# Kernel tuning notes

Hardware: AMD Instinct MI355X
Metric: run time of the kernel (lower is better)

## Reference

```python
import jax, jax.numpy as jnp
import numpy as np

B, N, C_IN, C_OUT = 2, 163842, 64, 64  # icosphere level-7 vertex count
K = 7  # 1-ring neighborhood size (center + 6 neighbors)


def setup_inputs() -> dict:
    key = jax.random.key(0)
    kx, kw, kb, kn = jax.random.split(key, 4)
    x = jax.random.normal(kx, (B, N, C_IN), dtype=jnp.float32)
    # nn.Linear(7*in_feats, out_feats): W is (out, 7*in), bias (out,)
    W = jax.random.normal(kw, (C_OUT, K * C_IN), dtype=jnp.float32) * (1.0 / np.sqrt(K * C_IN))
    b = jax.random.normal(kb, (C_OUT,), dtype=jnp.float32) * 0.01
    neigh_orders = jax.random.randint(kn, (K * N,), 0, N, dtype=jnp.int64)
    return {"x": x, "W": W, "b": b, "neigh_orders": neigh_orders}


def reference(x, W, b, neigh_orders):
    # Faithful translation of onering_conv_layer_batch.forward:
    #   x: (B, N, C) -> permute -> (B, C, N)
    #   gather 7N indices on vertex axis -> (B, C, 7N)
    #   view -> (B, N, 7C)  (raw reshape of the (C, 7N) block, as in the torch code)
    #   Linear(7C -> out)
    Bb, Nn, Cc = x.shape
    xp = jnp.transpose(x, (0, 2, 1))            # (B, C, N)
    g = jnp.take(xp, neigh_orders, axis=2)      # (B, C, 7N)
    mat = g.reshape(Bb, Nn, K * Cc)             # (B, N, 7C)
    return jnp.einsum('bnk,ok->bno', mat, W) + b
```

## Files before the change

kernel.cpp:

```cpp
#include <hip/hip_runtime.h>

typedef short bf8_t __attribute__((ext_vector_type(8)));
typedef float f32x4 __attribute__((ext_vector_type(4)));

static constexpr int Bc      = 2;
static constexpr int Nv      = 163842;
static constexpr int CIN     = 64;
static constexpr int COUT    = 64;
static constexpr int KK      = 448;
static constexpr int SEVEN_N = 7 * Nv;
static constexpr int THREADS = 512;

static constexpr int LM      = 3 * KK;
static constexpr int MST     = LM + KK;
static constexpr int NT      = (SEVEN_N + LM - 1) / LM;
static constexpr int NPAIR   = MST / 2;
static constexpr int CST     = 1352;
static constexpr int TILE_SH = 16 * CST;
static constexpr int TILE_AL = 27840;

__device__ inline unsigned pack2_bf16(float a, float b) {
    unsigned ua = __builtin_bit_cast(unsigned, a);
    unsigned ub = __builtin_bit_cast(unsigned, b);
    ua = (ua + 0x7FFFu + ((ua >> 16) & 1u)) >> 16;
    ub = (ub + 0x7FFFu + ((ub >> 16) & 1u));
    return (ua & 0xFFFFu) | (ub & 0xFFFF0000u);
}

__global__ __launch_bounds__(256) void xconv(const float* __restrict__ x,
                                             short* __restrict__ xb, int n) {
    const int i = (blockIdx.x * 256 + threadIdx.x) * 8;
    if (i >= n) return;
    const float4 a = *(const float4*)(x + i);
    const float4 c = *(const float4*)(x + i + 4);
    uint4 o;
    o.x = pack2_bf16(a.x, a.y); o.y = pack2_bf16(a.z, a.w);
    o.z = pack2_bf16(c.x, c.y); o.w = pack2_bf16(c.z, c.w);
    *(uint4*)(xb + i) = o;
}

__global__ __launch_bounds__(THREADS, 4) void conv_main_bf16(
    const short* __restrict__ xbf,
    const short* __restrict__ Wb,
    const float* __restrict__ bias,
    const int*   __restrict__ idx,
    float*       __restrict__ out)
{
    __shared__ short tile[TILE_AL];

    const int bid   = blockIdx.x;
    const int s     = bid & 7;
    const int b     = s & 1;
    const int mtres = s >> 1;
    const int rr    = bid >> 3;
    const int mt    = (rr >> 2) * 4 + mtres;
    const int cg    = rr & 3;
    if (mt >= NT) return;

    const int t    = threadIdx.x;
    const int M0   = mt * LM;
    const int mEnd = min(M0 + MST, SEVEN_N);
    const short* xb = xbf + (size_t)b * Nv * CIN;

    const int q     = t & 1;
    const int pidl  = t >> 1;
    const int choff = cg * 16 + q * 8;

    int d0a_[8];
    {
        int r448 = (int)(((unsigned)choff * (unsigned)SEVEN_N + (unsigned)M0) % 448u);
        #pragma unroll
        for (int j = 0; j < 8; ++j) {
            d0a_[j] = r448 ? 448 - r448 : 0;
            r448 += 14; if (r448 >= 448) r448 -= 448;
        }
    }

    int2 ivp[4];
    #pragma unroll
    for (int p = 0; p < 4; ++p) {
        const int pp = p * 256 + pidl;
        const int m0 = M0 + 2 * pp;
        if (pp < NPAIR && m0 + 1 < SEVEN_N) {
            ivp[p] = *(const int2*)(idx + m0);
        } else if (pp < NPAIR && m0 < SEVEN_N) {
            ivp[p].x = idx[m0]; ivp[p].y = idx[m0];
        } else {
            ivp[p].x = 0; ivp[p].y = 0;
        }
    }
    bf8_t v0[4], v1[4];
    #pragma unroll
    for (int p = 0; p < 4; ++p) {
        v0[p] = *(const bf8_t*)(xb + (size_t)ivp[p].x * CIN + choff);
        v1[p] = *(const bf8_t*)(xb + (size_t)ivp[p].y * CIN + choff);
    }

    const int lane = t & 63;
    const int w    = t >> 6;
    const int col  = lane & 15;
    const int hi   = lane >> 4;
    const int oc   = w & 3;
    const short* wbase = Wb + (oc * 16 + col) * KK + 8 * hi;
    bf8_t bfrag[14];
    #pragma unroll
    for (int k0 = 0; k0 < 14; ++k0)
        bfrag[k0] = *(const bf8_t*)(wbase + 32 * k0);

    #pragma unroll
    for (int p = 0; p < 4; ++p) {
        const int pp = p * 256 + pidl;
        const int m0 = M0 + 2 * pp;
        if (pp < NPAIR && m0 < mEnd) {
            const int dm = 2 * pp;
            #pragma unroll
            for (int j = 0; j < 8; ++j) {
                const int c  = q * 8 + j;
                const int pj = dm - d0a_[j];
                if ((unsigned)pj < (unsigned)LM) {
                    const unsigned lov = (unsigned short)v0[p][j];
                    const unsigned hiv = (unsigned short)v1[p][j];
                    *(unsigned*)&tile[c * CST + pj] = lov | (hiv << 16);
                }
            }
        }
    }
    __syncthreads();

    const short* abase0 = &tile[col * CST + 8 * hi];
    const float bo = bias[oc * 16 + col];

    for (int task = w; task < 12; task += 8) {
        const int r = task >> 2;
        const short* abase = abase0 + 448 * r;

        f32x4 acc = (f32x4){0.f, 0.f, 0.f, 0.f};
        #pragma unroll
        for (int k0 = 0; k0 < 14; ++k0) {
            const bf8_t afrag = *(const bf8_t*)(abase + 32 * k0);
            acc = __builtin_amdgcn_mfma_f32_16x16x32_bf16(afrag, bfrag[k0], acc, 0, 0, 0);
        }
        #pragma unroll
        for (int i = 0; i < 4; ++i) {
            const int c_s = 4 * hi + i;
            const int Cs  = cg * 16 + c_s;
            const int Ts  = Cs * SEVEN_N + M0;
            const int d0s = (448 - (Ts % 448)) % 448;
            const int sr  = M0 + d0s + 448 * r;
            if (sr + 448 <= SEVEN_N) {
                const int n = (Ts + d0s) / 448 + r;
                out[((size_t)b * Nv + n) * COUT + oc * 16 + col] = acc[i] + bo;
            }
        }
    }
}

static constexpr int STRIDE3 = 1800;
static constexpr int PPP     = THREADS / 4;
static constexpr int PASSES  = NPAIR / PPP;

__global__ __launch_bounds__(THREADS, 4) void conv_main_f32(
    const float* __restrict__ x,
    const short* __restrict__ Wb,
    const float* __restrict__ bias,
    const int*   __restrict__ idx,
    float*       __restrict__ out)
{
    __shared__ short tile[16 * STRIDE3];

    const int bid  = blockIdx.x;
    const int slot = bid & 7;
    const int cg   = slot >> 1;
    const int b    = slot & 1;
    const int mt   = bid >> 3;
    const int t    = threadIdx.x;
    const int M0   = mt * LM;
    const int mEnd = min(M0 + MST, SEVEN_N);
    const float* xb = x + (size_t)b * Nv * CIN;

    const int q    = t & 3;
    const int pidl = t >> 2;
    const int xoff = cg * 16 + q * 4;

    int iv0[PASSES], iv1[PASSES];
    #pragma unroll
    for (int p = 0; p < PASSES; ++p) {
        const int m0 = M0 + 2 * (p * PPP + pidl);
        const bool ok = (m0 < mEnd);
        iv0[p] = ok ? idx[m0] : 0;
        iv1[p] = (ok && m0 + 1 < mEnd) ? idx[m0 + 1] : 0;
    }
    float4 v0[PASSES], v1[PASSES];
    #pragma unroll
    for (int p = 0; p < PASSES; ++p) {
        v0[p] = *(const float4*)(xb + (size_t)iv0[p] * CIN + xoff);
        v1[p] = *(const float4*)(xb + (size_t)iv1[p] * CIN + xoff);
    }
    #pragma unroll
    for (int p = 0; p < PASSES; ++p) {
        const int m0 = M0 + 2 * (p * PPP + pidl);
        if (m0 < mEnd) {
            const float a0[4] = {v0[p].x, v0[p].y, v0[p].z, v0[p].w};
            const float a1[4] = {v1[p].x, v1[p].y, v1[p].z, v1[p].w};
            #pragma unroll
            for (int i = 0; i < 4; ++i) {
                const int c     = q * 4 + i;
                const int shift = (6 * c) & 7;
                const int ppos  = (m0 - M0) + shift;
                *(unsigned*)&tile[c * STRIDE3 + ppos] = pack2_bf16(a0[i], a1[i]);
            }
        }
    }
    __syncthreads();

    const int lane = t & 63;
    const int w    = t >> 6;
    const int col  = lane & 15;
    const int hi   = lane >> 4;
    const int oc   = w & 3;

    const short* wbase = Wb + (oc * 16 + col) * KK + 8 * hi;
    bf8_t bfrag[14];
    #pragma unroll
    for (int k0 = 0; k0 < 14; ++k0)
        bfrag[k0] = *(const bf8_t*)(wbase + 32 * k0);

    const int Ca  = cg * 16 + col;
    const int Ta  = Ca * SEVEN_N + M0;
    const int d0a = (448 - (Ta % 448)) % 448;
    const int sha = Ta & 7;
    const short* abase0 = &tile[col * STRIDE3 + d0a + sha + 8 * hi];
    const float bo = bias[oc * 16 + col];

    for (int task = w; task < 12; task += 8) {
        const int r = task >> 2;
        const short* abase = abase0 + 448 * r;
        f32x4 acc = (f32x4){0.f, 0.f, 0.f, 0.f};
        #pragma unroll
        for (int k0 = 0; k0 < 14; ++k0) {
            const bf8_t afrag = *(const bf8_t*)(abase + 32 * k0);
            acc = __builtin_amdgcn_mfma_f32_16x16x32_bf16(afrag, bfrag[k0], acc, 0, 0, 0);
        }
        #pragma unroll
        for (int i = 0; i < 4; ++i) {
            const int c_s = 4 * hi + i;
            const int Cs  = cg * 16 + c_s;
            const int Ts  = Cs * SEVEN_N + M0;
            const int d0s = (448 - (Ts % 448)) % 448;
            const int sr  = M0 + d0s + 448 * r;
            if (sr + 448 <= SEVEN_N) {
                const int n = (Ts + d0s) / 448 + r;
                out[((size_t)b * Nv + n) * COUT + oc * 16 + col] = acc[i] + bo;
            }
        }
    }
}

__global__ __launch_bounds__(256) void conv_cleanup(
    const float* __restrict__ x,
    const float* __restrict__ W,
    const float* __restrict__ bias,
    const int*   __restrict__ idx,
    float*       __restrict__ out)
{
    __shared__ float part[4][64];
    const int C = blockIdx.x;
    const int b = blockIdx.y;
    const int t = threadIdx.x;
    const int o = t & 63;
    const int p = t >> 6;
    const int n = (int)(((long long)(C + 1) * SEVEN_N + 447) / 448) - 1;
    const int s = 448 * n - C * SEVEN_N;
    if (s + 448 <= SEVEN_N) return;
    const float* xb = x + (size_t)b * Nv * CIN;
    float acc = 0.f;
    for (int j = p * 112; j < (p + 1) * 112; ++j) {
        int m = s + j, c = C;
        if (m >= SEVEN_N) { m -= SEVEN_N; c += 1; }
        acc += xb[(size_t)idx[m] * CIN + c] * W[o * KK + j];
    }
    part[p][o] = acc;
    __syncthreads();
    if (p == 0)
        out[((size_t)b * Nv + n) * COUT + o] =
            part[0][o] + part[1][o] + part[2][o] + part[3][o] + bias[o];
}

__global__ void wconv(const float* __restrict__ W, short* __restrict__ Wb) {
    const int i = blockIdx.x * 256 + threadIdx.x;
    if (i < COUT * KK) {
        unsigned u = __builtin_bit_cast(unsigned, W[i]);
        u = (u + 0x7FFFu + ((u >> 16) & 1u)) >> 16;
        Wb[i] = (short)u;
    }
}

extern "C" void kernel_launch(void* const* d_in, const int* in_sizes, int n_in,
                              void* d_out, int out_size, void* d_ws, size_t ws_size,
                              hipStream_t stream) {
    const float* x    = (const float*)d_in[0];
    const float* W    = (const float*)d_in[1];
    const float* bias = (const float*)d_in[2];
    const int*   idx  = (const int*)d_in[3];
    float*       out  = (float*)d_out;
    short*       Wb   = (short*)d_ws;

    hipLaunchKernelGGL(wconv, dim3((COUT * KK + 255) / 256), dim3(256), 0, stream, W, Wb);

    const int    nxe  = Bc * Nv * CIN;
    const size_t need = 65536 + (size_t)nxe * sizeof(short);
    if (ws_size >= need) {
        short* xbf = (short*)((char*)d_ws + 65536);
        hipLaunchKernelGGL(xconv, dim3((nxe / 8 + 255) / 256), dim3(256), 0, stream,
                           x, xbf, nxe);
        hipLaunchKernelGGL(conv_main_bf16, dim3(214 * 4 * 8), dim3(THREADS), 0, stream,
                           xbf, Wb, bias, idx, out);
    } else {
        hipLaunchKernelGGL(conv_main_f32, dim3(NT * 8), dim3(THREADS), 0, stream,
                           x, Wb, bias, idx, out);
    }
    hipLaunchKernelGGL(conv_cleanup, dim3(CIN, Bc), dim3(256), 0, stream,
                       x, W, bias, idx, out);
}
```

Measured before the change: 184.2 us.

## Make bf16 conv kernel persistent with software-pipelined gathers across tiles

Turns the one-tile-per-block bf16 kernel into a persistent kernel with 512 blocks, each stepping through M-tiles with a stride of 64. While MFMA work runs on the current tile, it prefetches the next tile's gathered activations and the index values for the tile after that. Per-row output offsets are precomputed once per block instead of being recomputed on every tile. This hides gather latency and cuts block launch overhead, at the cost of extra barriers, higher register pressure and reloading the weight fragments on every iteration.

```diff
diff --git a/kernel.cpp b/kernel.cpp
--- a/kernel.cpp
+++ b/kernel.cpp
@@ -16,8 +16,8 @@
 static constexpr int NT      = (SEVEN_N + LM - 1) / LM;
 static constexpr int NPAIR   = MST / 2;
 static constexpr int CST     = 1352;
-static constexpr int TILE_SH = 16 * CST;
 static constexpr int TILE_AL = 27840;
+static constexpr int MTSTEP  = 64;
 
 __device__ inline unsigned pack2_bf16(float a, float b) {
     unsigned ua = __builtin_bit_cast(unsigned, a);
@@ -52,14 +52,10 @@
     const int s     = bid & 7;
     const int b     = s & 1;
     const int mtres = s >> 1;
-    const int rr    = bid >> 3;
-    const int mt    = (rr >> 2) * 4 + mtres;
-    const int cg    = rr & 3;
-    if (mt >= NT) return;
-
-    const int t    = threadIdx.x;
-    const int M0   = mt * LM;
-    const int mEnd = min(M0 + MST, SEVEN_N);
+    const int r0    = bid >> 3;
+    const int cg    = r0 & 3;
+    const int mt0   = (r0 >> 2) * 4 + mtres;
+    const int t     = threadIdx.x;
     const short* xb = xbf + (size_t)b * Nv * CIN;
 
     const int q     = t & 1;
@@ -68,32 +64,12 @@
 
     int d0a_[8];
     {
-        int r448 = (int)(((unsigned)choff * (unsigned)SEVEN_N + (unsigned)M0) % 448u);
+        int r448 = (int)(((unsigned)choff * (unsigned)SEVEN_N) % 448u);
         #pragma unroll
         for (int j = 0; j < 8; ++j) {
             d0a_[j] = r448 ? 448 - r448 : 0;
             r448 += 14; if (r448 >= 448) r448 -= 448;
         }
-    }
-
-    int2 ivp[4];
-    #pragma unroll
-    for (int p = 0; p < 4; ++p) {
-        const int pp = p * 256 + pidl;
-        const int m0 = M0 + 2 * pp;
-        if (pp < NPAIR && m0 + 1 < SEVEN_N) {
-            ivp[p] = *(const int2*)(idx + m0);
-        } else if (pp < NPAIR && m0 < SEVEN_N) {
-            ivp[p].x = idx[m0]; ivp[p].y = idx[m0];
-        } else {
-            ivp[p].x = 0; ivp[p].y = 0;
-        }
-    }
-    bf8_t v0[4], v1[4];
-    #pragma unroll
-    for (int p = 0; p < 4; ++p) {
-        v0[p] = *(const bf8_t*)(xb + (size_t)ivp[p].x * CIN + choff);
-        v1[p] = *(const bf8_t*)(xb + (size_t)ivp[p].y * CIN + choff);
     }
 
     const int lane = t & 63;
@@ -102,56 +78,154 @@
     const int hi   = lane >> 4;
     const int oc   = w & 3;
     const short* wbase = Wb + (oc * 16 + col) * KK + 8 * hi;
-    bf8_t bfrag[14];
-    #pragma unroll
-    for (int k0 = 0; k0 < 14; ++k0)
-        bfrag[k0] = *(const bf8_t*)(wbase + 32 * k0);
-
+    const float bo = bias[oc * 16 + col];
+
+    int d0s_[4], nb_[4];
+    #pragma unroll
+    for (int i = 0; i < 4; ++i) {
+        const int Cs = cg * 16 + 4 * hi + i;
+        const int Ts = (int)(((long long)Cs * SEVEN_N) % 448);
+        d0s_[i] = Ts ? 448 - Ts : 0;
+        nb_[i]  = (int)(((long long)Cs * SEVEN_N + d0s_[i]) / 448);
+    }
+
+    if (mt0 >= NT) return;
+
+    int mt = mt0;
+    int M0 = mt * LM;
+
+    int2 ivC[4];
     #pragma unroll
     for (int p = 0; p < 4; ++p) {
         const int pp = p * 256 + pidl;
         const int m0 = M0 + 2 * pp;
-        if (pp < NPAIR && m0 < mEnd) {
-            const int dm = 2 * pp;
-            #pragma unroll
-            for (int j = 0; j < 8; ++j) {
-                const int c  = q * 8 + j;
-                const int pj = dm - d0a_[j];
-                if ((unsigned)pj < (unsigned)LM) {
-                    const unsigned lov = (unsigned short)v0[p][j];
-                    const unsigned hiv = (unsigned short)v1[p][j];
-                    *(unsigned*)&tile[c * CST + pj] = lov | (hiv << 16);
+        if (pp < NPAIR && m0 + 1 < SEVEN_N)      ivC[p] = *(const int2*)(idx + m0);
+        else if (pp < NPAIR && m0 < SEVEN_N)   { ivC[p].x = idx[m0]; ivC[p].y = idx[m0]; }
+        else                                   { ivC[p].x = 0; ivC[p].y = 0; }
+    }
+    bf8_t v0[4], v1[4];
+    #pragma unroll
+    for (int p = 0; p < 4; ++p) {
+        v0[p] = *(const bf8_t*)(xb + (size_t)ivC[p].x * CIN + choff);
+        v1[p] = *(const bf8_t*)(xb + (size_t)ivC[p].y * CIN + choff);
+    }
+    int  mtN = mt + MTSTEP;
+    bool vN  = (mtN < NT);
+    int2 ivN[4];
+    #pragma unroll
+    for (int p = 0; p < 4; ++p) { ivN[p].x = 0; ivN[p].y = 0; }
+    if (vN) {
+        const int MN = mtN * LM;
+        #pragma unroll
+        for (int p = 0; p < 4; ++p) {
+            const int pp = p * 256 + pidl;
+            const int m0 = MN + 2 * pp;
+            if (pp < NPAIR && m0 + 1 < SEVEN_N)      ivN[p] = *(const int2*)(idx + m0);
+            else if (pp < NPAIR && m0 < SEVEN_N)   { ivN[p].x = idx[m0]; ivN[p].y = idx[m0]; }
+        }
+    }
+    {
+        const int mEnd = min(M0 + MST, SEVEN_N);
+        #pragma unroll
+        for (int p = 0; p < 4; ++p) {
+            const int pp = p * 256 + pidl;
+            const int m0 = M0 + 2 * pp;
+            if (pp < NPAIR && m0 < mEnd) {
+                const int dm = 2 * pp;
+                #pragma unroll
+                for (int j = 0; j < 8; ++j) {
+                    const int c  = q * 8 + j;
+                    const int pj = dm - d0a_[j];
+                    if ((unsigned)pj < (unsigned)LM) {
+                        const unsigned lov = (unsigned short)v0[p][j];
+                        const unsigned hiv = (unsigned short)v1[p][j];
+                        *(unsigned*)&tile[c * CST + pj] = lov | (hiv << 16);
+                    }
                 }
             }
         }
     }
     __syncthreads();
 
-    const short* abase0 = &tile[col * CST + 8 * hi];
-    const float bo = bias[oc * 16 + col];
-
-    for (int task = w; task < 12; task += 8) {
-        const int r = task >> 2;
-        const short* abase = abase0 + 448 * r;
-
-        f32x4 acc = (f32x4){0.f, 0.f, 0.f, 0.f};
-        #pragma unroll
-        for (int k0 = 0; k0 < 14; ++k0) {
-            const bf8_t afrag = *(const bf8_t*)(abase + 32 * k0);
-            acc = __builtin_amdgcn_mfma_f32_16x16x32_bf16(afrag, bfrag[k0], acc, 0, 0, 0);
-        }
-        #pragma unroll
-        for (int i = 0; i < 4; ++i) {
-            const int c_s = 4 * hi + i;
-            const int Cs  = cg * 16 + c_s;
-            const int Ts  = Cs * SEVEN_N + M0;
-            const int d0s = (448 - (Ts % 448)) % 448;
-            const int sr  = M0 + d0s + 448 * r;
-            if (sr + 448 <= SEVEN_N) {
-                const int n = (Ts + d0s) / 448 + r;
-                out[((size_t)b * Nv + n) * COUT + oc * 16 + col] = acc[i] + bo;
-            }
-        }
+    while (true) {
+        bf8_t bfr[14];
+        #pragma unroll
+        for (int k0 = 0; k0 < 14; ++k0)
+            bfr[k0] = *(const bf8_t*)(wbase + 32 * k0);
+
+        bf8_t n0[4], n1[4];
+        if (vN) {
+            #pragma unroll
+            for (int p = 0; p < 4; ++p) {
+                n0[p] = *(const bf8_t*)(xb + (size_t)ivN[p].x * CIN + choff);
+                n1[p] = *(const bf8_t*)(xb + (size_t)ivN[p].y * CIN + choff);
+            }
+        }
+        const int  mtN2 = mtN + MTSTEP;
+        const bool vN2  = vN && (mtN2 < NT);
+        int2 ivN2[4];
+        #pragma unroll
+        for (int p = 0; p < 4; ++p) { ivN2[p].x = 0; ivN2[p].y = 0; }
+        if (vN2) {
+            const int MN2 = mtN2 * LM;
+            #pragma unroll
+            for (int p = 0; p < 4; ++p) {
+                const int pp = p * 256 + pidl;
+                const int m0 = MN2 + 2 * pp;
+                if (pp < NPAIR && m0 + 1 < SEVEN_N)      ivN2[p] = *(const int2*)(idx + m0);
+                else if (pp < NPAIR && m0 < SEVEN_N)   { ivN2[p].x = idx[m0]; ivN2[p].y = idx[m0]; }
+            }
+        }
+        __builtin_amdgcn_sched_barrier(0);
+
+        for (int task = w; task < 12; task += 8) {
+            const int r = task >> 2;
+            const short* abase = &tile[col * CST + 448 * r + 8 * hi];
+            f32x4 acc = (f32x4){0.f, 0.f, 0.f, 0.f};
+            #pragma unroll
+            for (int k0 = 0; k0 < 14; ++k0) {
+                const bf8_t afrag = *(const bf8_t*)(abase + 32 * k0);
+                acc = __builtin_amdgcn_mfma_f32_16x16x32_bf16(afrag, bfr[k0], acc, 0, 0, 0);
+            }
+            #pragma unroll
+            for (int i = 0; i < 4; ++i) {
+                const int sr = M0 + d0s_[i] + 448 * r;
+                if (sr + 448 <= SEVEN_N) {
+                    const int n = nb_[i] + mt * 3 + r;
+                    out[((size_t)b * Nv + n) * COUT + oc * 16 + col] = acc[i] + bo;
+                }
+            }
+        }
+
+        if (!vN) break;
+        __syncthreads();
+
+        mt = mtN; M0 = mt * LM;
+        {
+            const int mEnd = min(M0 + MST, SEVEN_N);
+            #pragma unroll
+            for (int p = 0; p < 4; ++p) {
+                const int pp = p * 256 + pidl;
+                const int m0 = M0 + 2 * pp;
+                if (pp < NPAIR && m0 < mEnd) {
+                    const int dm = 2 * pp;
+                    #pragma unroll
+                    for (int j = 0; j < 8; ++j) {
+                        const int c  = q * 8 + j;
+                        const int pj = dm - d0a_[j];
+                        if ((unsigned)pj < (unsigned)LM) {
+                            const unsigned lov = (unsigned short)n0[p][j];
+                            const unsigned hiv = (unsigned short)n1[p][j];
+                            *(unsigned*)&tile[c * CST + pj] = lov | (hiv << 16);
+                        }
+                    }
+                }
+            }
+        }
+        #pragma unroll
+        for (int p = 0; p < 4; ++p) ivN[p] = ivN2[p];
+        mtN = mtN2; vN = vN2;
+        __syncthreads();
     }
 }
 
@@ -313,7 +387,7 @@
         short* xbf = (short*)((char*)d_ws + 65536);
         hipLaunchKernelGGL(xconv, dim3((nxe / 8 + 255) / 256), dim3(256), 0, stream,
                            x, xbf, nxe);
-        hipLaunchKernelGGL(conv_main_bf16, dim3(214 * 4 * 8), dim3(THREADS), 0, stream,
+        hipLaunchKernelGGL(conv_main_bf16, dim3(512), dim3(THREADS), 0, stream,
                            xbf, Wb, bias, idx, out);
     } else {
         hipLaunchKernelGGL(conv_main_f32, dim3(NT * 8), dim3(THREADS), 0, stream,
```

New measurement: 256.4 us. 1.39x slower.

## Store bf16 activations in per-channel-group planar layout for compact gathers

Applied to the files above, without the earlier changes.

The bf16 conversion kernel now writes x into a layout split by batch and 16-channel group, so each vertex's 16 channels form one contiguous 32-byte record per group. The main kernel gathers from that plane, so each block touches a working set a quarter the size, which should improve L2/MALL hit rates for the random neighbor gathers. It also reverts the interleaved block-to-tile mapping to a simple bid>>3 scheme. It shrinks the LDS tile to the exact size and raises the launch-bounds occupancy hint from 4 to 6, which may force register spilling.

```diff
diff --git a/kernel.cpp b/kernel.cpp
--- a/kernel.cpp
+++ b/kernel.cpp
@@ -17,7 +17,6 @@
 static constexpr int NPAIR   = MST / 2;
 static constexpr int CST     = 1352;
 static constexpr int TILE_SH = 16 * CST;
-static constexpr int TILE_AL = 27840;
 
 __device__ inline unsigned pack2_bf16(float a, float b) {
     unsigned ua = __builtin_bit_cast(unsigned, a);
@@ -27,48 +26,51 @@
     return (ua & 0xFFFFu) | (ub & 0xFFFF0000u);
 }
 
-__global__ __launch_bounds__(256) void xconv(const float* __restrict__ x,
-                                             short* __restrict__ xb, int n) {
-    const int i = (blockIdx.x * 256 + threadIdx.x) * 8;
-    if (i >= n) return;
-    const float4 a = *(const float4*)(x + i);
-    const float4 c = *(const float4*)(x + i + 4);
+__global__ __launch_bounds__(256) void xperm(const float* __restrict__ x,
+                                             short* __restrict__ xp) {
+    const int u = blockIdx.x * 256 + threadIdx.x;
+    if (u >= Bc * Nv * 8) return;
+    const int b   = (u >= Nv * 8) ? 1 : 0;
+    const int rem = u - b * Nv * 8;
+    const int v   = rem >> 3;
+    const int oct = rem & 7;
+    const float* src = x + ((size_t)(b * Nv + v) * CIN + oct * 8);
+    const float4 a = *(const float4*)(src);
+    const float4 c = *(const float4*)(src + 4);
     uint4 o;
     o.x = pack2_bf16(a.x, a.y); o.y = pack2_bf16(a.z, a.w);
     o.z = pack2_bf16(c.x, c.y); o.w = pack2_bf16(c.z, c.w);
-    *(uint4*)(xb + i) = o;
-}
-
-__global__ __launch_bounds__(THREADS, 4) void conv_main_bf16(
-    const short* __restrict__ xbf,
+    short* dst = xp + ((size_t)((b * 4 + (oct >> 1)) * Nv + v) * 16 + (oct & 1) * 8);
+    *(uint4*)dst = o;
+}
+
+__global__ __launch_bounds__(THREADS, 6) void conv_main_bf16(
+    const short* __restrict__ xp,
     const short* __restrict__ Wb,
     const float* __restrict__ bias,
     const int*   __restrict__ idx,
     float*       __restrict__ out)
 {
-    __shared__ short tile[TILE_AL];
-
-    const int bid   = blockIdx.x;
-    const int s     = bid & 7;
-    const int b     = s & 1;
-    const int mtres = s >> 1;
-    const int rr    = bid >> 3;
-    const int mt    = (rr >> 2) * 4 + mtres;
-    const int cg    = rr & 3;
-    if (mt >= NT) return;
+    __shared__ short tile[TILE_SH];
+
+    const int bid = blockIdx.x;
+    const int s   = bid & 7;
+    const int cg  = s >> 1;
+    const int b   = s & 1;
+    const int mt  = bid >> 3;
 
     const int t    = threadIdx.x;
     const int M0   = mt * LM;
     const int mEnd = min(M0 + MST, SEVEN_N);
-    const short* xb = xbf + (size_t)b * Nv * CIN;
+    const short* xs = xp + (size_t)(b * 4 + cg) * Nv * 16;
 
     const int q     = t & 1;
     const int pidl  = t >> 1;
-    const int choff = cg * 16 + q * 8;
+    const int chb   = cg * 16 + q * 8;
 
     int d0a_[8];
     {
-        int r448 = (int)(((unsigned)choff * (unsigned)SEVEN_N + (unsigned)M0) % 448u);
+        int r448 = (int)(((unsigned)chb * (unsigned)SEVEN_N + (unsigned)M0) % 448u);
         #pragma unroll
         for (int j = 0; j < 8; ++j) {
             d0a_[j] = r448 ? 448 - r448 : 0;
@@ -92,8 +94,8 @@
     bf8_t v0[4], v1[4];
     #pragma unroll
     for (int p = 0; p < 4; ++p) {
-        v0[p] = *(const bf8_t*)(xb + (size_t)ivp[p].x * CIN + choff);
-        v1[p] = *(const bf8_t*)(xb + (size_t)ivp[p].y * CIN + choff);
+        v0[p] = *(const bf8_t*)(xs + (size_t)ivp[p].x * 16 + q * 8);
+        v1[p] = *(const bf8_t*)(xs + (size_t)ivp[p].y * 16 + q * 8);
     }
 
     const int lane = t & 63;
@@ -310,11 +312,12 @@
     const int    nxe  = Bc * Nv * CIN;
     const size_t need = 65536 + (size_t)nxe * sizeof(short);
     if (ws_size >= need) {
-        short* xbf = (short*)((char*)d_ws + 65536);
-        hipLaunchKernelGGL(xconv, dim3((nxe / 8 + 255) / 256), dim3(256), 0, stream,
-                           x, xbf, nxe);
-        hipLaunchKernelGGL(conv_main_bf16, dim3(214 * 4 * 8), dim3(THREADS), 0, stream,
-                           xbf, Wb, bias, idx, out);
+        short* xp = (short*)((char*)d_ws + 65536);
+        const int nunits = Bc * Nv * 8;
+        hipLaunchKernelGGL(xperm, dim3((nunits + 255) / 256), dim3(256), 0, stream,
+                           x, xp);
+        hipLaunchKernelGGL(conv_main_bf16, dim3(NT * 8), dim3(THREADS), 0, stream,
+                           xp, Wb, bias, idx, out);
     } else {
         hipLaunchKernelGGL(conv_main_f32, dim3(NT * 8), dim3(THREADS), 0, stream,
                            x, Wb, bias, idx, out);
```

Measured after the change: 414.0 us. +124.8%, slower.
